# Kernel optimization log

Measured on AMD Instinct MI355X. Metric: run time of the kernel, lower is better.

## Reference

```python
import jax, jax.numpy as jnp
import numpy as np

N_NODES = 10000
N_EDGES = 160000
IN_FEAT = 1024
H_FEAT = 1024
NUM_CLASSES = 64


def setup_inputs() -> dict:
    key = jax.random.key(0)
    ks = jax.random.split(key, 8)
    h = jax.random.normal(ks[0], (N_NODES, IN_FEAT), dtype=jnp.float32)
    src = jax.random.randint(ks[1], (N_EDGES,), 0, N_NODES, dtype=jnp.int32)
    dst = jax.random.randint(ks[2], (N_EDGES,), 0, N_NODES, dtype=jnp.int32)
    # Xavier-ish scaled weights (DGL uses xavier_uniform for GraphConv)
    W1 = jax.random.normal(ks[3], (IN_FEAT, H_FEAT), dtype=jnp.float32) * (1.0 / np.sqrt(IN_FEAT))
    b1 = jnp.zeros((H_FEAT,), dtype=jnp.float32)
    W2 = jax.random.normal(ks[4], (H_FEAT, H_FEAT), dtype=jnp.float32) * (1.0 / np.sqrt(H_FEAT))
    b2 = jnp.zeros((H_FEAT,), dtype=jnp.float32)
    W3 = jax.random.normal(ks[5], (H_FEAT, NUM_CLASSES), dtype=jnp.float32) * (1.0 / np.sqrt(H_FEAT))
    b3 = jnp.zeros((NUM_CLASSES,), dtype=jnp.float32)
    return {"h": h, "src": src, "dst": dst,
            "W1": W1, "b1": b1, "W2": W2, "b2": b2, "W3": W3, "b3": b3}


def _graph_conv(src, dst, norm_src, norm_dst, x, W, b):
    """DGL GraphConv with norm='both':
    out = D_dst^{-1/2} * sum_{(u,v) in E} (D_src^{-1/2} * x)_u  @ W + b
    """
    xs = x * norm_src[:, None]                     # [N, d] scaled source feats
    msg = xs[src]                                  # [E, d] gather
    agg = jax.ops.segment_sum(msg, dst, num_segments=N_NODES)  # [N, d] scatter-add
    agg = agg * norm_dst[:, None]
    return agg @ W + b


def reference(h, src, dst, W1, b1, W2, b2, W3, b3):
    ones = jnp.ones((N_EDGES,), dtype=jnp.float32)
    deg_out = jax.ops.segment_sum(ones, src, num_segments=N_NODES)  # out-degree of src
    deg_in = jax.ops.segment_sum(ones, dst, num_segments=N_NODES)   # in-degree of dst
    norm_src = jnp.clip(deg_out, 1.0, None) ** -0.5
    norm_dst = jnp.clip(deg_in, 1.0, None) ** -0.5

    x = _graph_conv(src, dst, norm_src, norm_dst, h, W1, b1)
    x = jax.nn.relu(x)
    x = _graph_conv(src, dst, norm_src, norm_dst, x, W2, b2)
    x = jax.nn.relu(x)
    x = _graph_conv(src, dst, norm_src, norm_dst, x, W3, b3)
    return x
```

## Files before the change

kernel.cpp:

```cpp
#include <hip/hip_runtime.h>

constexpr int NN   = 10000;
constexpr int NE   = 160000;
constexpr int F    = 1024;
constexpr int C3   = 64;
constexpr int MPAD = 10240;

typedef __attribute__((ext_vector_type(8))) short short8;
typedef __attribute__((ext_vector_type(8))) unsigned short ushort8v;
typedef __attribute__((ext_vector_type(4))) float floatx4;

__device__ __forceinline__ unsigned short f2bf(float f) {
    union { float f; unsigned u; } v; v.f = f;
    unsigned r = v.u + 0x7fff + ((v.u >> 16) & 1);
    return (unsigned short)(r >> 16);
}
__device__ __forceinline__ float bf2f(unsigned short u) {
    union { unsigned u; float f; } v; v.u = ((unsigned)u) << 16;
    return v.f;
}

__device__ __forceinline__ void gl_lds16(const void* g, void* l) {
    __builtin_amdgcn_global_load_lds(
        (const __attribute__((address_space(1))) unsigned int*)g,
        (__attribute__((address_space(3))) unsigned int*)l, 16, 0, 0);
}


__global__ __launch_bounds__(256) void k_degree(const int* __restrict__ src,
                                                const int* __restrict__ dst,
                                                int* __restrict__ deg_out,
                                                int* __restrict__ deg_in) {
    int e = blockIdx.x * 256 + threadIdx.x;
    if (e < NE) {
        atomicAdd(&deg_out[src[e]], 1);
        atomicAdd(&deg_in[dst[e]], 1);
    }
}

__global__ __launch_bounds__(1024) void k_scan(const int* __restrict__ deg_in,
                                               const int* __restrict__ deg_out,
                                               int* __restrict__ row_ptr,
                                               int* __restrict__ cursor,
                                               float* __restrict__ norm_src,
                                               float* __restrict__ norm_dst) {
    constexpr int CH = 10;
    __shared__ int sums[1024];
    const int tid = threadIdx.x;
    int local[CH];
    int tsum = 0;
#pragma unroll
    for (int j = 0; j < CH; ++j) {
        int idx = tid * CH + j;
        int v = (idx < NN) ? deg_in[idx] : 0;
        local[j] = v;
        tsum += v;
        if (idx < MPAD) {
            norm_src[idx] = rsqrtf(fmaxf((float)deg_out[idx], 1.0f));
            norm_dst[idx] = rsqrtf(fmaxf((float)deg_in[idx], 1.0f));
        }
    }
    sums[tid] = tsum;
    __syncthreads();
    for (int off = 1; off < 1024; off <<= 1) {
        int v = (tid >= off) ? sums[tid - off] : 0;
        __syncthreads();
        sums[tid] += v;
        __syncthreads();
    }
    int run = sums[tid] - tsum;
#pragma unroll
    for (int j = 0; j < CH; ++j) {
        int idx = tid * CH + j;
        if (idx < NN) {
            row_ptr[idx] = run;
            cursor[idx]  = run;
        }
        run += local[j];
    }
    if (tid == 1023) row_ptr[NN] = sums[1023];
}

__global__ __launch_bounds__(256) void k_bucket(const int* __restrict__ src,
                                                const int* __restrict__ dst,
                                                int* __restrict__ cursor,
                                                int* __restrict__ csr_src) {
    int e = blockIdx.x * 256 + threadIdx.x;
    if (e < NE) {
        int slot = atomicAdd(&cursor[dst[e]], 1);
        csr_src[slot] = src[e];
    }
}

__global__ __launch_bounds__(256) void k_wconv_all(const float* __restrict__ W1,
                                                   const float* __restrict__ W2,
                                                   const float* __restrict__ W3,
                                                   unsigned short* __restrict__ Wt1,
                                                   unsigned short* __restrict__ Wt2,
                                                   unsigned short* __restrict__ Wt3) {
    __shared__ float tile[32][33];
    const float* W; unsigned short* Wt; int N, n0, k0;
    int b = blockIdx.x;
    if (b < 1024)      { W = W1; Wt = Wt1; N = F;  n0 = (b & 31) * 32;          k0 = (b >> 5) * 32; }
    else if (b < 2048) { b -= 1024; W = W2; Wt = Wt2; N = F;  n0 = (b & 31) * 32; k0 = (b >> 5) * 32; }
    else               { b -= 2048; W = W3; Wt = Wt3; N = C3; n0 = (b & 1) * 32;  k0 = (b >> 1) * 32; }
    const int tx = threadIdx.x & 31, ty = threadIdx.x >> 5;
#pragma unroll
    for (int i = 0; i < 32; i += 8)
        tile[ty + i][tx] = W[(size_t)(k0 + ty + i) * N + n0 + tx];
    __syncthreads();
#pragma unroll
    for (int i = 0; i < 32; i += 8)
        Wt[(size_t)(n0 + ty + i) * F + k0 + tx] = f2bf(tile[tx][ty + i]);
}


__global__ __launch_bounds__(256) void k_hcvt(const float* __restrict__ h,
                                              const float* __restrict__ norm_src,
                                              unsigned short* __restrict__ hb) {
    int idx = blockIdx.x * 256 + threadIdx.x;
    int v = idx >> 7, f8 = (idx & 127) * 8;
    float ns = norm_src[v];
    const float4 a = *(const float4*)(h + (size_t)v * F + f8);
    const float4 b = *(const float4*)(h + (size_t)v * F + f8 + 4);
    ushort8v o;
    o[0] = f2bf(ns * a.x); o[1] = f2bf(ns * a.y);
    o[2] = f2bf(ns * a.z); o[3] = f2bf(ns * a.w);
    o[4] = f2bf(ns * b.x); o[5] = f2bf(ns * b.y);
    o[6] = f2bf(ns * b.z); o[7] = f2bf(ns * b.w);
    *(ushort8v*)(hb + (size_t)v * F + f8) = o;
}

__global__ __launch_bounds__(256) void k_aggb(const unsigned short* __restrict__ xb,
                                              const int* __restrict__ row_ptr,
                                              const int* __restrict__ csr_src,
                                              unsigned short* __restrict__ aggb) {
    const int c = blockIdx.x & 7;
    const int g = blockIdx.x >> 3;
    const int v = g * 16 + (threadIdx.x >> 4);
    const int f8 = c * 128 + (threadIdx.x & 15) * 8;
    const unsigned short* xr = xb + f8;
    const int lo = row_ptr[v], hi = row_ptr[v + 1];
    float acc[8] = {0.f, 0.f, 0.f, 0.f, 0.f, 0.f, 0.f, 0.f};
    int i = lo;
    for (; i + 8 <= hi; i += 8) {
        int s0 = csr_src[i],     s1 = csr_src[i + 1];
        int s2 = csr_src[i + 2], s3 = csr_src[i + 3];
        int s4 = csr_src[i + 4], s5 = csr_src[i + 5];
        int s6 = csr_src[i + 6], s7 = csr_src[i + 7];
        ushort8v x0 = *(const ushort8v*)(xr + (size_t)s0 * F);
        ushort8v x1 = *(const ushort8v*)(xr + (size_t)s1 * F);
        ushort8v x2 = *(const ushort8v*)(xr + (size_t)s2 * F);
        ushort8v x3 = *(const ushort8v*)(xr + (size_t)s3 * F);
        ushort8v x4 = *(const ushort8v*)(xr + (size_t)s4 * F);
        ushort8v x5 = *(const ushort8v*)(xr + (size_t)s5 * F);
        ushort8v x6 = *(const ushort8v*)(xr + (size_t)s6 * F);
        ushort8v x7 = *(const ushort8v*)(xr + (size_t)s7 * F);
#pragma unroll
        for (int j = 0; j < 8; ++j) acc[j] += bf2f(x0[j]);
#pragma unroll
        for (int j = 0; j < 8; ++j) acc[j] += bf2f(x1[j]);
#pragma unroll
        for (int j = 0; j < 8; ++j) acc[j] += bf2f(x2[j]);
#pragma unroll
        for (int j = 0; j < 8; ++j) acc[j] += bf2f(x3[j]);
#pragma unroll
        for (int j = 0; j < 8; ++j) acc[j] += bf2f(x4[j]);
#pragma unroll
        for (int j = 0; j < 8; ++j) acc[j] += bf2f(x5[j]);
#pragma unroll
        for (int j = 0; j < 8; ++j) acc[j] += bf2f(x6[j]);
#pragma unroll
        for (int j = 0; j < 8; ++j) acc[j] += bf2f(x7[j]);
    }
    if (i + 4 <= hi) {
        int s0 = csr_src[i],     s1 = csr_src[i + 1];
        int s2 = csr_src[i + 2], s3 = csr_src[i + 3];
        ushort8v x0 = *(const ushort8v*)(xr + (size_t)s0 * F);
        ushort8v x1 = *(const ushort8v*)(xr + (size_t)s1 * F);
        ushort8v x2 = *(const ushort8v*)(xr + (size_t)s2 * F);
        ushort8v x3 = *(const ushort8v*)(xr + (size_t)s3 * F);
#pragma unroll
        for (int j = 0; j < 8; ++j) acc[j] += bf2f(x0[j]);
#pragma unroll
        for (int j = 0; j < 8; ++j) acc[j] += bf2f(x1[j]);
#pragma unroll
        for (int j = 0; j < 8; ++j) acc[j] += bf2f(x2[j]);
#pragma unroll
        for (int j = 0; j < 8; ++j) acc[j] += bf2f(x3[j]);
        i += 4;
    }
    for (; i < hi; ++i) {
        int s = csr_src[i];
        ushort8v xv = *(const ushort8v*)(xr + (size_t)s * F);
#pragma unroll
        for (int j = 0; j < 8; ++j) acc[j] += bf2f(xv[j]);
    }
    ushort8v o;
#pragma unroll
    for (int j = 0; j < 8; ++j) o[j] = f2bf(acc[j]);
    *(ushort8v*)(aggb + (size_t)v * F + f8) = o;
}

__global__ __launch_bounds__(256) void k_agg64(const float* __restrict__ z,
                                               const int* __restrict__ row_ptr,
                                               const int* __restrict__ csr_src,
                                               const float* __restrict__ norm_dst,
                                               const float* __restrict__ b3,
                                               float* __restrict__ out) {
    const int v = blockIdx.x * 16 + (threadIdx.x >> 4);
    if (v >= NN) return;
    const int f4 = (threadIdx.x & 15) * 4;
    const int lo = row_ptr[v], hi = row_ptr[v + 1];
    float4 acc = {0.f, 0.f, 0.f, 0.f};
    int i = lo;
    for (; i + 4 <= hi; i += 4) {
        int s0 = csr_src[i],     s1 = csr_src[i + 1];
        int s2 = csr_src[i + 2], s3 = csr_src[i + 3];
        float4 z0 = *(const float4*)(z + (size_t)s0 * C3 + f4);
        float4 z1 = *(const float4*)(z + (size_t)s1 * C3 + f4);
        float4 z2 = *(const float4*)(z + (size_t)s2 * C3 + f4);
        float4 z3v = *(const float4*)(z + (size_t)s3 * C3 + f4);
        acc.x += z0.x + z1.x + z2.x + z3v.x;
        acc.y += z0.y + z1.y + z2.y + z3v.y;
        acc.z += z0.z + z1.z + z2.z + z3v.z;
        acc.w += z0.w + z1.w + z2.w + z3v.w;
    }
    for (; i < hi; ++i) {
        int s = csr_src[i];
        float4 zv = *(const float4*)(z + (size_t)s * C3 + f4);
        acc.x += zv.x; acc.y += zv.y; acc.z += zv.z; acc.w += zv.w;
    }
    float nd = norm_dst[v];
    float4 bv = *(const float4*)(b3 + f4);
    float4 o;
    o.x = acc.x * nd + bv.x; o.y = acc.y * nd + bv.y;
    o.z = acc.z * nd + bv.z; o.w = acc.w * nd + bv.w;
    *(float4*)(out + (size_t)v * C3 + f4) = o;
}

__global__ __launch_bounds__(512) void k_gemm_bf16(
        const unsigned short* __restrict__ A,
        const unsigned short* __restrict__ Bt,
        const float* __restrict__ bias,
        const float* __restrict__ rs1,
        const float* __restrict__ rs2,
        unsigned short* __restrict__ Cb) {
    __shared__ short As[2][128 * 32];
    __shared__ short Bs[2][128 * 32];
    const int t = threadIdx.x, lane = t & 63, wid = t >> 6;
    const int j = blockIdx.x >> 3;
    const int m0 = ((blockIdx.x & 7) * 10 + (j >> 3)) * 128;
    const int n0 = (j & 7) * 128;
    const int wm0 = (wid & 1) * 64, wn0 = (wid >> 1) * 32;
    const int lr = lane & 15, q = lane >> 4;

    const int rS  = wid * 16 + (lane >> 2);
    const int sS  = (((lane & 3) ^ ((rS >> 1) & 3)) * 8);
    const unsigned short* aSrc = A  + (size_t)(m0 + rS) * F + sS;
    const unsigned short* bSrc = Bt + (size_t)(n0 + rS) * F + sS;
    short* aDst = &As[0][wid * 512];
    short* bDst = &Bs[0][wid * 512];

    const short* ap[4];
    const short* bp[2];
#pragma unroll
    for (int mb = 0; mb < 4; ++mb) {
        int m = wm0 + mb * 16 + lr;
        ap[mb] = &As[0][m * 32 + (q ^ ((m >> 1) & 3)) * 8];
    }
#pragma unroll
    for (int nb = 0; nb < 2; ++nb) {
        int n = wn0 + nb * 16 + lr;
        bp[nb] = &Bs[0][n * 32 + (q ^ ((n >> 1) & 3)) * 8];
    }

    floatx4 acc[4][2] = {};

    gl_lds16(aSrc, aDst);
    gl_lds16(bSrc, bDst);

    for (int kt = 0; kt < F / 32; ++kt) {
        const int buf = kt & 1;
        __syncthreads();
        if (kt + 1 < F / 32) {
            int k0 = (kt + 1) * 32;
            gl_lds16(aSrc + k0, aDst + (buf ^ 1) * (128 * 32));
            gl_lds16(bSrc + k0, bDst + (buf ^ 1) * (128 * 32));
        }
        const int bo = buf * (128 * 32);
        short8 af[4], bf[2];
#pragma unroll
        for (int mb = 0; mb < 4; ++mb) af[mb] = *(const short8*)(ap[mb] + bo);
#pragma unroll
        for (int nb = 0; nb < 2; ++nb) bf[nb] = *(const short8*)(bp[nb] + bo);
#pragma unroll
        for (int mb = 0; mb < 4; ++mb)
#pragma unroll
            for (int nb = 0; nb < 2; ++nb)
                acc[mb][nb] = __builtin_amdgcn_mfma_f32_16x16x32_bf16(
                    af[mb], bf[nb], acc[mb][nb], 0, 0, 0);
    }

    float s1[4][4], s2[4][4];
#pragma unroll
    for (int mb = 0; mb < 4; ++mb)
#pragma unroll
        for (int r = 0; r < 4; ++r) {
            int row = m0 + wm0 + mb * 16 + q * 4 + r;
            s1[mb][r] = rs1[row];
            s2[mb][r] = rs2[row];
        }
#pragma unroll
    for (int nb = 0; nb < 2; ++nb) {
        int col = n0 + wn0 + nb * 16 + lr;
        float bv = bias[col];
#pragma unroll
        for (int mb = 0; mb < 4; ++mb)
#pragma unroll
            for (int r = 0; r < 4; ++r) {
                int row = m0 + wm0 + mb * 16 + q * 4 + r;
                float v = fmaxf(acc[mb][nb][r] * s1[mb][r] + bv, 0.f) * s2[mb][r];
                Cb[(size_t)row * F + col] = f2bf(v);
            }
    }
}

__global__ __launch_bounds__(256) void k_gemm3(
        const unsigned short* __restrict__ A,
        const unsigned short* __restrict__ Bt,
        float* __restrict__ Z) {
    __shared__ short As3[2][64 * 32];
    __shared__ short Bs3[2][64 * 32];
    const int t = threadIdx.x, lane = t & 63, wid = t >> 6;
    const int m0 = blockIdx.x * 64;
    const int lr = lane & 15, q = lane >> 4;

    const int r = wid * 16 + (lane >> 2);
    const int soff = (((lane & 3) ^ ((r >> 1) & 3)) * 8);
    const unsigned short* aSrc = A  + (size_t)(m0 + r) * F + soff;
    const unsigned short* bSrc = Bt + (size_t)r * F + soff;

    const short* ap;
    {
        int m = wid * 16 + lr;
        ap = &As3[0][m * 32 + (q ^ ((m >> 1) & 3)) * 8];
    }
    const short* bp[4];
#pragma unroll
    for (int nb = 0; nb < 4; ++nb) {
        int n = nb * 16 + lr;
        bp[nb] = &Bs3[0][n * 32 + (q ^ ((n >> 1) & 3)) * 8];
    }

    floatx4 acc[4] = {};

    gl_lds16(aSrc, &As3[0][wid * 512]);
    gl_lds16(bSrc, &Bs3[0][wid * 512]);

    for (int kt = 0; kt < F / 32; ++kt) {
        const int buf = kt & 1;
        __syncthreads();
        if (kt + 1 < F / 32) {
            int k0 = (kt + 1) * 32;
            gl_lds16(aSrc + k0, &As3[buf ^ 1][wid * 512]);
            gl_lds16(bSrc + k0, &Bs3[buf ^ 1][wid * 512]);
        }
        const int bo = buf * (64 * 32);
        short8 af = *(const short8*)(ap + bo);
        short8 bf[4];
#pragma unroll
        for (int nb = 0; nb < 4; ++nb) bf[nb] = *(const short8*)(bp[nb] + bo);
#pragma unroll
        for (int nb = 0; nb < 4; ++nb)
            acc[nb] = __builtin_amdgcn_mfma_f32_16x16x32_bf16(af, bf[nb], acc[nb], 0, 0, 0);
    }

#pragma unroll
    for (int nb = 0; nb < 4; ++nb) {
        int col = nb * 16 + lr;
#pragma unroll
        for (int ri = 0; ri < 4; ++ri) {
            int row = m0 + wid * 16 + q * 4 + ri;
            Z[(size_t)row * C3 + col] = acc[nb][ri];
        }
    }
}


extern "C" void kernel_launch(void* const* d_in, const int* in_sizes, int n_in,
                              void* d_out, int out_size, void* d_ws, size_t ws_size,
                              hipStream_t stream) {
    const float* h   = (const float*)d_in[0];
    const int*   src = (const int*)d_in[1];
    const int*   dst = (const int*)d_in[2];
    const float* W1  = (const float*)d_in[3];
    const float* b1  = (const float*)d_in[4];
    const float* W2  = (const float*)d_in[5];
    const float* b2  = (const float*)d_in[6];
    const float* W3  = (const float*)d_in[7];
    const float* b3  = (const float*)d_in[8];
    float* out = (float*)d_out;

    char* ws = (char*)d_ws;
    int*   deg_out  = (int*)ws;                       ws += MPAD * 4;
    int*   deg_in   = (int*)ws;                       ws += MPAD * 4;
    float* norm_src = (float*)ws;                     ws += MPAD * 4;
    float* norm_dst = (float*)ws;                     ws += MPAD * 4;
    int*   row_ptr  = (int*)ws;                       ws += (NN + 1) * 4;
    int*   cursor   = (int*)ws;                       ws += NN * 4;
    int*   csr_src  = (int*)ws;                       ws += NE * 4;
    ws = (char*)(((size_t)ws + 255) & ~(size_t)255);
    unsigned short* hb   = (unsigned short*)ws;       ws += (size_t)MPAD * F * 2;
    unsigned short* aggb = (unsigned short*)ws;       ws += (size_t)MPAD * F * 2;
    unsigned short* xb   = (unsigned short*)ws;       ws += (size_t)MPAD * F * 2;
    unsigned short* Wt1  = (unsigned short*)ws;       ws += (size_t)F * F * 2;
    unsigned short* Wt2  = (unsigned short*)ws;       ws += (size_t)F * F * 2;
    unsigned short* Wt3  = (unsigned short*)ws;       ws += (size_t)C3 * F * 2;
    float* z3       = (float*)ws;

    hipMemsetAsync(deg_out, 0, 2 * MPAD * sizeof(int), stream);
    k_degree<<<(NE + 255) / 256, 256, 0, stream>>>(src, dst, deg_out, deg_in);
    k_scan<<<1, 1024, 0, stream>>>(deg_in, deg_out, row_ptr, cursor, norm_src, norm_dst);
    k_bucket<<<(NE + 255) / 256, 256, 0, stream>>>(src, dst, cursor, csr_src);
    k_wconv_all<<<2112, 256, 0, stream>>>(W1, W2, W3, Wt1, Wt2, Wt3);
    k_hcvt<<<NN * 128 / 256, 256, 0, stream>>>(h, norm_src, hb);

    k_aggb<<<(NN / 16) * 8, 256, 0, stream>>>(hb, row_ptr, csr_src, aggb);
    k_gemm_bf16<<<(MPAD / 128) * (F / 128), 512, 0, stream>>>(aggb, Wt1, b1, norm_dst, norm_src, xb);

    k_aggb<<<(NN / 16) * 8, 256, 0, stream>>>(xb, row_ptr, csr_src, aggb);
    k_gemm_bf16<<<(MPAD / 128) * (F / 128), 512, 0, stream>>>(aggb, Wt2, b2, norm_dst, norm_src, xb);

    k_gemm3<<<MPAD / 64, 256, 0, stream>>>(xb, Wt3, z3);
    k_agg64<<<(NN + 15) / 16, 256, 0, stream>>>(z3, row_ptr, csr_src, norm_dst, b3, out);
}
```

Baseline: 277.7 us.

## Split aggregation edges across two half-warps and widen GEMM tile to 256 columns

The bf16 aggregation kernel now assigns two 16-thread groups per destination node, each taking alternating edges, and combines them with a cross-lane shuffle before one group writes the result. This doubles the memory-level parallelism of the gather for nodes with about 16 edges. Separately, the main GEMM block tile grows from 128x128 to 128x256, with each wave computing a 64x64 sub-tile. That improves reuse of the A tile and the ratio of MFMA work to LDS reads, at the cost of more accumulator registers, twice the B shared memory, and half as many blocks.

```diff
diff --git a/kernel.cpp b/kernel.cpp
--- a/kernel.cpp
+++ b/kernel.cpp
@@ -137,17 +137,18 @@
                                               unsigned short* __restrict__ aggb) {
     const int c = blockIdx.x & 7;
     const int g = blockIdx.x >> 3;
-    const int v = g * 16 + (threadIdx.x >> 4);
+    const int v = g * 8 + (threadIdx.x >> 5);
+    const int half = (threadIdx.x >> 4) & 1;
     const int f8 = c * 128 + (threadIdx.x & 15) * 8;
     const unsigned short* xr = xb + f8;
     const int lo = row_ptr[v], hi = row_ptr[v + 1];
     float acc[8] = {0.f, 0.f, 0.f, 0.f, 0.f, 0.f, 0.f, 0.f};
-    int i = lo;
-    for (; i + 8 <= hi; i += 8) {
-        int s0 = csr_src[i],     s1 = csr_src[i + 1];
-        int s2 = csr_src[i + 2], s3 = csr_src[i + 3];
-        int s4 = csr_src[i + 4], s5 = csr_src[i + 5];
-        int s6 = csr_src[i + 6], s7 = csr_src[i + 7];
+    int i = lo + half;
+    for (; i + 14 < hi; i += 16) {
+        int s0 = csr_src[i],      s1 = csr_src[i + 2];
+        int s2 = csr_src[i + 4],  s3 = csr_src[i + 6];
+        int s4 = csr_src[i + 8],  s5 = csr_src[i + 10];
+        int s6 = csr_src[i + 12], s7 = csr_src[i + 14];
         ushort8v x0 = *(const ushort8v*)(xr + (size_t)s0 * F);
         ushort8v x1 = *(const ushort8v*)(xr + (size_t)s1 * F);
         ushort8v x2 = *(const ushort8v*)(xr + (size_t)s2 * F);
@@ -173,9 +174,9 @@
 #pragma unroll
         for (int j = 0; j < 8; ++j) acc[j] += bf2f(x7[j]);
     }
-    if (i + 4 <= hi) {
-        int s0 = csr_src[i],     s1 = csr_src[i + 1];
-        int s2 = csr_src[i + 2], s3 = csr_src[i + 3];
+    if (i + 6 < hi) {
+        int s0 = csr_src[i],     s1 = csr_src[i + 2];
+        int s2 = csr_src[i + 4], s3 = csr_src[i + 6];
         ushort8v x0 = *(const ushort8v*)(xr + (size_t)s0 * F);
         ushort8v x1 = *(const ushort8v*)(xr + (size_t)s1 * F);
         ushort8v x2 = *(const ushort8v*)(xr + (size_t)s2 * F);
@@ -188,18 +189,32 @@
         for (int j = 0; j < 8; ++j) acc[j] += bf2f(x2[j]);
 #pragma unroll
         for (int j = 0; j < 8; ++j) acc[j] += bf2f(x3[j]);
+        i += 8;
+    }
+    if (i + 2 < hi) {
+        int s0 = csr_src[i], s1 = csr_src[i + 2];
+        ushort8v x0 = *(const ushort8v*)(xr + (size_t)s0 * F);
+        ushort8v x1 = *(const ushort8v*)(xr + (size_t)s1 * F);
+#pragma unroll
+        for (int j = 0; j < 8; ++j) acc[j] += bf2f(x0[j]);
+#pragma unroll
+        for (int j = 0; j < 8; ++j) acc[j] += bf2f(x1[j]);
         i += 4;
     }
-    for (; i < hi; ++i) {
+    if (i < hi) {
         int s = csr_src[i];
         ushort8v xv = *(const ushort8v*)(xr + (size_t)s * F);
 #pragma unroll
         for (int j = 0; j < 8; ++j) acc[j] += bf2f(xv[j]);
     }
-    ushort8v o;
-#pragma unroll
-    for (int j = 0; j < 8; ++j) o[j] = f2bf(acc[j]);
-    *(ushort8v*)(aggb + (size_t)v * F + f8) = o;
+#pragma unroll
+    for (int j = 0; j < 8; ++j) acc[j] += __shfl_xor(acc[j], 16);
+    if (half == 0) {
+        ushort8v o;
+#pragma unroll
+        for (int j = 0; j < 8; ++j) o[j] = f2bf(acc[j]);
+        *(ushort8v*)(aggb + (size_t)v * F + f8) = o;
+    }
 }
 
 __global__ __launch_bounds__(256) void k_agg64(const float* __restrict__ z,
@@ -247,12 +262,12 @@
         const float* __restrict__ rs2,
         unsigned short* __restrict__ Cb) {
     __shared__ short As[2][128 * 32];
-    __shared__ short Bs[2][128 * 32];
+    __shared__ short Bs[2][256 * 32];
     const int t = threadIdx.x, lane = t & 63, wid = t >> 6;
     const int j = blockIdx.x >> 3;
-    const int m0 = ((blockIdx.x & 7) * 10 + (j >> 3)) * 128;
-    const int n0 = (j & 7) * 128;
-    const int wm0 = (wid & 1) * 64, wn0 = (wid >> 1) * 32;
+    const int m0 = ((blockIdx.x & 7) * 10 + (j >> 2)) * 128;
+    const int n0 = (j & 3) * 256;
+    const int wm0 = (wid & 1) * 64, wn0 = (wid >> 1) * 64;
     const int lr = lane & 15, q = lane >> 4;
 
     const int rS  = wid * 16 + (lane >> 2);
@@ -263,22 +278,23 @@
     short* bDst = &Bs[0][wid * 512];
 
     const short* ap[4];
-    const short* bp[2];
+    const short* bp[4];
 #pragma unroll
     for (int mb = 0; mb < 4; ++mb) {
         int m = wm0 + mb * 16 + lr;
         ap[mb] = &As[0][m * 32 + (q ^ ((m >> 1) & 3)) * 8];
     }
 #pragma unroll
-    for (int nb = 0; nb < 2; ++nb) {
+    for (int nb = 0; nb < 4; ++nb) {
         int n = wn0 + nb * 16 + lr;
         bp[nb] = &Bs[0][n * 32 + (q ^ ((n >> 1) & 3)) * 8];
     }
 
-    floatx4 acc[4][2] = {};
+    floatx4 acc[4][4] = {};
 
     gl_lds16(aSrc, aDst);
     gl_lds16(bSrc, bDst);
+    gl_lds16(bSrc + 128 * F, bDst + 128 * 32);
 
     for (int kt = 0; kt < F / 32; ++kt) {
         const int buf = kt & 1;
@@ -286,18 +302,19 @@
         if (kt + 1 < F / 32) {
             int k0 = (kt + 1) * 32;
             gl_lds16(aSrc + k0, aDst + (buf ^ 1) * (128 * 32));
-            gl_lds16(bSrc + k0, bDst + (buf ^ 1) * (128 * 32));
-        }
-        const int bo = buf * (128 * 32);
-        short8 af[4], bf[2];
-#pragma unroll
-        for (int mb = 0; mb < 4; ++mb) af[mb] = *(const short8*)(ap[mb] + bo);
-#pragma unroll
-        for (int nb = 0; nb < 2; ++nb) bf[nb] = *(const short8*)(bp[nb] + bo);
+            gl_lds16(bSrc + k0, bDst + (buf ^ 1) * (256 * 32));
+            gl_lds16(bSrc + 128 * F + k0, bDst + 128 * 32 + (buf ^ 1) * (256 * 32));
+        }
+        const int aBo = buf * (128 * 32), bBo = buf * (256 * 32);
+        short8 af[4], bf[4];
+#pragma unroll
+        for (int mb = 0; mb < 4; ++mb) af[mb] = *(const short8*)(ap[mb] + aBo);
+#pragma unroll
+        for (int nb = 0; nb < 4; ++nb) bf[nb] = *(const short8*)(bp[nb] + bBo);
 #pragma unroll
         for (int mb = 0; mb < 4; ++mb)
 #pragma unroll
-            for (int nb = 0; nb < 2; ++nb)
+            for (int nb = 0; nb < 4; ++nb)
                 acc[mb][nb] = __builtin_amdgcn_mfma_f32_16x16x32_bf16(
                     af[mb], bf[nb], acc[mb][nb], 0, 0, 0);
     }
@@ -312,7 +329,7 @@
             s2[mb][r] = rs2[row];
         }
 #pragma unroll
-    for (int nb = 0; nb < 2; ++nb) {
+    for (int nb = 0; nb < 4; ++nb) {
         int col = n0 + wn0 + nb * 16 + lr;
         float bv = bias[col];
 #pragma unroll
@@ -426,11 +443,11 @@
     k_wconv_all<<<2112, 256, 0, stream>>>(W1, W2, W3, Wt1, Wt2, Wt3);
     k_hcvt<<<NN * 128 / 256, 256, 0, stream>>>(h, norm_src, hb);
 
-    k_aggb<<<(NN / 16) * 8, 256, 0, stream>>>(hb, row_ptr, csr_src, aggb);
-    k_gemm_bf16<<<(MPAD / 128) * (F / 128), 512, 0, stream>>>(aggb, Wt1, b1, norm_dst, norm_src, xb);
-
-    k_aggb<<<(NN / 16) * 8, 256, 0, stream>>>(xb, row_ptr, csr_src, aggb);
-    k_gemm_bf16<<<(MPAD / 128) * (F / 128), 512, 0, stream>>>(aggb, Wt2, b2, norm_dst, norm_src, xb);
+    k_aggb<<<(NN / 8) * 8, 256, 0, stream>>>(hb, row_ptr, csr_src, aggb);
+    k_gemm_bf16<<<(MPAD / 128) * (F / 256), 512, 0, stream>>>(aggb, Wt1, b1, norm_dst, norm_src, xb);
+
+    k_aggb<<<(NN / 8) * 8, 256, 0, stream>>>(xb, row_ptr, csr_src, aggb);
+    k_gemm_bf16<<<(MPAD / 128) * (F / 256), 512, 0, stream>>>(aggb, Wt2, b2, norm_dst, norm_src, xb);
 
     k_gemm3<<<MPAD / 64, 256, 0, stream>>>(xb, Wt3, z3);
     k_agg64<<<(NN + 15) / 16, 256, 0, stream>>>(z3, row_ptr, csr_src, norm_dst, b3, out);
```

New measurement: 292.4 us. 1.05x slower.

## Triple-buffer GEMM LDS loads with partial vmcnt waits; drop 4-way agg tail

Applied to the files above, without the earlier changes.

The bf16 GEMM moves from double to triple buffering of the A/B tiles in LDS and keeps two k-tiles of global-to-LDS loads in flight. The full __syncthreads is replaced by an explicit s_waitcnt vmcnt(2) plus a raw barrier, and the k-loop is fully unrolled. The goal is to hide global load latency behind the MFMA work. This raises LDS use per block, which may lower occupancy, and it relies on hand-counted outstanding loads. Separately, the aggregation kernel drops its 4-edge remainder step, so leftover edges go through the scalar loop.

```diff
diff --git a/kernel.cpp b/kernel.cpp
--- a/kernel.cpp
+++ b/kernel.cpp
@@ -173,23 +173,6 @@
 #pragma unroll
         for (int j = 0; j < 8; ++j) acc[j] += bf2f(x7[j]);
     }
-    if (i + 4 <= hi) {
-        int s0 = csr_src[i],     s1 = csr_src[i + 1];
-        int s2 = csr_src[i + 2], s3 = csr_src[i + 3];
-        ushort8v x0 = *(const ushort8v*)(xr + (size_t)s0 * F);
-        ushort8v x1 = *(const ushort8v*)(xr + (size_t)s1 * F);
-        ushort8v x2 = *(const ushort8v*)(xr + (size_t)s2 * F);
-        ushort8v x3 = *(const ushort8v*)(xr + (size_t)s3 * F);
-#pragma unroll
-        for (int j = 0; j < 8; ++j) acc[j] += bf2f(x0[j]);
-#pragma unroll
-        for (int j = 0; j < 8; ++j) acc[j] += bf2f(x1[j]);
-#pragma unroll
-        for (int j = 0; j < 8; ++j) acc[j] += bf2f(x2[j]);
-#pragma unroll
-        for (int j = 0; j < 8; ++j) acc[j] += bf2f(x3[j]);
-        i += 4;
-    }
     for (; i < hi; ++i) {
         int s = csr_src[i];
         ushort8v xv = *(const ushort8v*)(xr + (size_t)s * F);
@@ -246,8 +229,8 @@
         const float* __restrict__ rs1,
         const float* __restrict__ rs2,
         unsigned short* __restrict__ Cb) {
-    __shared__ short As[2][128 * 32];
-    __shared__ short Bs[2][128 * 32];
+    __shared__ short As[3][128 * 32];
+    __shared__ short Bs[3][128 * 32];
     const int t = threadIdx.x, lane = t & 63, wid = t >> 6;
     const int j = blockIdx.x >> 3;
     const int m0 = ((blockIdx.x & 7) * 10 + (j >> 3)) * 128;
@@ -277,18 +260,27 @@
 
     floatx4 acc[4][2] = {};
 
-    gl_lds16(aSrc, aDst);
-    gl_lds16(bSrc, bDst);
-
+    gl_lds16(aSrc,      aDst);
+    gl_lds16(bSrc,      bDst);
+    gl_lds16(aSrc + 32, aDst + 4096);
+    gl_lds16(bSrc + 32, bDst + 4096);
+
+#pragma unroll
     for (int kt = 0; kt < F / 32; ++kt) {
-        const int buf = kt & 1;
-        __syncthreads();
-        if (kt + 1 < F / 32) {
-            int k0 = (kt + 1) * 32;
-            gl_lds16(aSrc + k0, aDst + (buf ^ 1) * (128 * 32));
-            gl_lds16(bSrc + k0, bDst + (buf ^ 1) * (128 * 32));
-        }
-        const int bo = buf * (128 * 32);
+        if (kt < F / 32 - 1) {
+            asm volatile("s_waitcnt vmcnt(2)" ::: "memory");
+        } else {
+            asm volatile("s_waitcnt vmcnt(0)" ::: "memory");
+        }
+        __builtin_amdgcn_s_barrier();
+        __builtin_amdgcn_sched_barrier(0);
+        if (kt + 2 < F / 32) {
+            const int k0 = (kt + 2) * 32;
+            const int bb = ((kt + 2) % 3) * 4096;
+            gl_lds16(aSrc + k0, aDst + bb);
+            gl_lds16(bSrc + k0, bDst + bb);
+        }
+        const int bo = (kt % 3) * 4096;
         short8 af[4], bf[2];
 #pragma unroll
         for (int mb = 0; mb < 4; ++mb) af[mb] = *(const short8*)(ap[mb] + bo);
```

Result: slower. 292.2 us (+5.2%).
